# Kernel optimization log

Measured on AMD Instinct MI355X. Metric: run time of the kernel, lower is better.

Reference implementation:

```python
import jax, jax.numpy as jnp
import numpy as np

B, H, W = 16, 180, 240  # dim=(180,240), batch inferred from last event in torch code
N = 8_000_000


def setup_inputs() -> dict:
    key = jax.random.key(0)
    k0, k1, k2, k3, k4 = jax.random.split(key, 5)
    x = jax.random.randint(k0, (N,), 0, W).astype(jnp.float32)
    y = jax.random.randint(k1, (N,), 0, H).astype(jnp.float32)
    t = jax.random.uniform(k2, (N,), dtype=jnp.float32)
    p = (jax.random.randint(k3, (N,), 0, 2) * 2 - 1).astype(jnp.float32)  # polarity in {-1,1}
    # b sorted so events[-1,-1] == B-1, matching how torch code infers B
    b = jnp.sort(jax.random.randint(k4, (N,), 0, B)).astype(jnp.float32)
    events = jnp.stack([x, y, t, p, b], axis=1)  # [N,5]
    return {"events": events}


def reference(events):
    x, y, t, p, b = (events[:, i] for i in range(5))
    bi = b.astype(jnp.int32)

    # per-batch time normalization: t /= max(t within batch)
    tmax = jax.ops.segment_max(t, bi, num_segments=B)
    t = t / tmax[bi]
    p = (p + 1.0) / 2.0  # computed (as in torch) but unused downstream

    # full-res event-count histogram: idx = x + W*y + W*H*b
    idx_c = (x + W * y + W * H * b).astype(jnp.int32)
    container = jnp.zeros(B * H * W, jnp.int32).at[idx_c].add(1, mode="drop")
    container = container.reshape(B, H, W)

    # half-res counter/timer; replicate torch float floordiv exactly:
    # idx = x//2 + (W*y)//4 + (W*H*b)//4
    idx_k = (jnp.floor_divide(x, 2.0)
             + jnp.floor_divide(W * y, 4.0)
             + jnp.floor_divide(W * H * b, 4.0)).astype(jnp.int32)
    nvox = B * (H // 2) * (W // 2)
    counter = jnp.zeros(nvox, jnp.int32).at[idx_k].add(1, mode="drop").astype(jnp.float32)
    timer = jnp.zeros(nvox, jnp.float32).at[idx_k].add(t, mode="drop")
    timer = timer / jnp.where(counter == 0, 1.0, counter)  # mean timestamp per voxel
    counter = counter.reshape(B, H // 2, W // 2)
    timer = timer.reshape(B, H // 2, W // 2)

    # strided diffs on the full-res histogram
    dy = container[:, ::2] - container[:, 1::2]          # [B, H/2, W]
    diff_y = dy[:, :, ::2] + dy[:, :, 1::2]              # [B, H/2, W/2]
    dx = container[:, :, ::2] - container[:, :, 1::2]    # [B, H, W/2]
    diff_x = dx[:, 1::2] + dx[:, ::2]                    # [B, H/2, W/2]

    return container, counter, timer, diff_x, diff_y
```

## Files before the change

### kernel.cpp

```cpp
#include <hip/hip_runtime.h>
#include <stdint.h>

constexpr int NB    = 16;
constexpr int NH    = 180;
constexpr int NW    = 240;
constexpr int FULL  = NB * NH * NW;
constexpr int SEG   = (NH / 2) * (NW / 2);
constexpr int HALF  = NB * SEG;
constexpr int CELLS = NH * NW;
constexpr int H4W   = CELLS / 8;
constexpr int EVT   = 512;
constexpr int NBPB  = 32;
constexpr int NBLK  = NB * NBPB;
constexpr int RT    = 43;

constexpr int O_TMAX  = 0;
constexpr int O_CONT  = 16;
constexpr int O_TSUM  = O_CONT + FULL;
constexpr int O_BLEED = O_TSUM + HALF;
constexpr int ZERO_WORDS = O_BLEED + HALF;
constexpr int O_BND   = ZERO_WORDS;
constexpr int O_PRIV  = O_BND + 32;
constexpr int O_CNTFB = ZERO_WORDS;

__global__ __launch_bounds__(256) void k_init(unsigned int* __restrict__ ws, int bound) {
    int i = blockIdx.x * blockDim.x + threadIdx.x;
    int stride = gridDim.x * blockDim.x;
    for (; i < bound; i += stride) ws[i] = 0u;
}

__global__ __launch_bounds__(64) void k_bounds(const float* __restrict__ ev, int n,
                                               int* __restrict__ bnd) {
    int b = threadIdx.x;
    if (b > NB) return;
    int lo = 0, hi = n;
    while (lo < hi) {
        int mid = (lo + hi) >> 1;
        float v = ev[(size_t)5 * mid + 4];
        if (v < (float)b) lo = mid + 1; else hi = mid;
    }
    bnd[b] = lo;
}

__global__ __launch_bounds__(EVT) void k_merged(const float* __restrict__ ev,
                                                const int* __restrict__ bnd,
                                                unsigned int* __restrict__ ws,
                                                unsigned int* __restrict__ h4p,
                                                float* __restrict__ tsp) {
    unsigned int* tmaxb   = ws + O_TMAX;
    float*        bleed_g = (float*)(ws + O_BLEED);

    __shared__ unsigned int h4[H4W];
    __shared__ float        ts[SEG];
    __shared__ unsigned int bsm;
    int tid = threadIdx.x;
    for (int i = tid; i < H4W; i += EVT) h4[i] = 0u;
    for (int i = tid; i < SEG; i += EVT) ts[i] = 0.0f;
    if (tid == 0) bsm = 0u;

    int b0 = blockIdx.x >> 5;
    int r  = blockIdx.x & (NBPB - 1);
    int sb = bnd[b0], eb = bnd[b0 + 1];
    long long len = (long long)(eb - sb);
    int s = sb + (int)(len * r / NBPB);
    int e = sb + (int)(len * (r + 1) / NBPB);
    __syncthreads();

    float tloc = 0.0f;

    auto proc = [&](float fx, float fy, float t) {
        int xi = (int)fx, yi = (int)fy;
        int cell = xi + NW * yi;
        int loc  = (xi >> 1) + (NW / 4) * yi;
        tloc = fmaxf(tloc, t);
        atomicAdd(&h4[cell >> 3], 1u << ((cell & 7) * 4));
        if (loc < SEG) {
            atomicAdd(&ts[loc], t);
        } else {
            int ik = SEG * b0 + loc;
            if (ik < HALF) atomicAdd(&bleed_g[ik], t);
        }
    };

    if (s < e) {
        int as_ = min((s + 3) & ~3, e);
        for (int i = s + tid; i < as_; i += EVT) {
            const float* rr = ev + (size_t)5 * i;
            proc(rr[0], rr[1], rr[2]);
        }
        int ng = (e - as_) >> 2;
        const float4* e4 = (const float4*)ev;
        size_t qbase = (size_t)5 * (size_t)(as_ >> 2);
        for (int g = tid; g < ng; g += 2 * EVT) {
            int g2 = g + EVT;
            size_t qb = qbase + (size_t)5 * g;
            float4 q0 = e4[qb], q1 = e4[qb + 1], q2 = e4[qb + 2],
                   q3 = e4[qb + 3], q4 = e4[qb + 4];
            if (g2 < ng) {
                size_t qc = qbase + (size_t)5 * g2;
                float4 p0 = e4[qc], p1 = e4[qc + 1], p2 = e4[qc + 2],
                       p3 = e4[qc + 3], p4 = e4[qc + 4];
                proc(q0.x, q0.y, q0.z);
                proc(q1.y, q1.z, q1.w);
                proc(q2.z, q2.w, q3.x);
                proc(q3.w, q4.x, q4.y);
                proc(p0.x, p0.y, p0.z);
                proc(p1.y, p1.z, p1.w);
                proc(p2.z, p2.w, p3.x);
                proc(p3.w, p4.x, p4.y);
            } else {
                proc(q0.x, q0.y, q0.z);
                proc(q1.y, q1.z, q1.w);
                proc(q2.z, q2.w, q3.x);
                proc(q3.w, q4.x, q4.y);
            }
        }
        for (int i = as_ + (ng << 2) + tid; i < e; i += EVT) {
            const float* rr = ev + (size_t)5 * i;
            proc(rr[0], rr[1], rr[2]);
        }
    }

#pragma unroll
    for (int o = 32; o > 0; o >>= 1) tloc = fmaxf(tloc, __shfl_xor(tloc, o));
    if ((tid & 63) == 0) atomicMax(&bsm, __float_as_uint(tloc));
    __syncthreads();

    unsigned int* dh = h4p + (size_t)blockIdx.x * H4W;
    for (int i = tid; i < H4W; i += EVT) dh[i] = h4[i];
    float* dt = tsp + (size_t)blockIdx.x * SEG;
    for (int i = tid; i < SEG; i += EVT) dt[i] = ts[i];
    if (tid == 0 && bsm) atomicMax(&tmaxb[b0], bsm);
}

__global__ __launch_bounds__(256) void k_reduce(const unsigned int* __restrict__ ws,
                                                const unsigned int* __restrict__ h4p,
                                                const float* __restrict__ tsp,
                                                float* __restrict__ out) {
    const unsigned int* tmaxb   = ws + O_TMAX;
    const float*        bleed_g = (const float*)(ws + O_BLEED);

    int tid  = threadIdx.x;
    int b    = blockIdx.x / RT;
    int tile = blockIdx.x - b * RT;

    int rem = tile * 256 + tid;
    if (rem >= SEG) return;
    int v = b * SEG + rem;
    int i = rem / (NW / 2);
    int j = rem - i * (NW / 2);
    int cbl = 480 * i + 2 * j;
    int cbg = CELLS * b + cbl;

    unsigned c00 = 0, c01 = 0, c10 = 0, c11 = 0, oc = 0;
    float tsum = 0.0f;

    bool prev = false;
    int ocell;
    if (j >= 60)      ocell = cbl + 120;
    else if (i >= 1)  ocell = cbl - 120;
    else { prev = true; ocell = 43080 + 2 * j; }

    int w0i = cbl >> 3, nib = (cbl & 7) * 4;
    int w1i = w0i + 30;
    int owi = ocell >> 3, onib = (ocell & 7) * 4;

    int base = b << 5;
#pragma unroll 8
    for (int k = 0; k < NBPB; ++k) {
        const unsigned int* hp = h4p + (size_t)(base + k) * H4W;
        unsigned w0 = hp[w0i], w1 = hp[w1i], wo = hp[owi];
        float tv = tsp[(size_t)(base + k) * SEG + rem];
        c00 += (w0 >> nib) & 15u;  c01 += (w0 >> (nib + 4)) & 15u;
        c10 += (w1 >> nib) & 15u;  c11 += (w1 >> (nib + 4)) & 15u;
        oc  += ((wo >> onib) & 15u) + ((wo >> (onib + 4)) & 15u);
        tsum += tv;
    }
    if (prev) {
        oc = 0;
        if (b >= 1) {
            int pb = (b - 1) << 5;
#pragma unroll 8
            for (int k = 0; k < NBPB; ++k) {
                unsigned wo = h4p[(size_t)(pb + k) * H4W + owi];
                oc += ((wo >> onib) & 15u) + ((wo >> (onib + 4)) & 15u);
            }
        }
    }
    unsigned cnt = c00 + c01 + oc;

    out[cbg]          = (float)c00;
    out[cbg + 1]      = (float)c01;
    out[cbg + NW]     = (float)c10;
    out[cbg + NW + 1] = (float)c11;
    out[FULL + v] = (float)cnt;

    float tm = __uint_as_float(tmaxb[b]);
    if (!(tm > 0.0f)) tm = 1.0f;
    float tmp = (b > 0) ? __uint_as_float(tmaxb[b - 1]) : 1.0f;
    if (!(tmp > 0.0f)) tmp = 1.0f;
    float s = tsum / tm + bleed_g[v] / tmp;
    out[FULL + HALF + v] = s / (float)(cnt == 0 ? 1u : cnt);

    out[FULL + 2 * HALF + v] = (float)((int)c00 - (int)c01 + (int)c10 - (int)c11);
    out[FULL + 3 * HALF + v] = (float)((int)c00 + (int)c01 - (int)c10 - (int)c11);
}


__global__ __launch_bounds__(256) void f_events(const float* __restrict__ ev, int n,
                                                unsigned int* __restrict__ ws) {
    unsigned int* tmaxb = ws + O_TMAX;
    int*   cont  = (int*)(ws + O_CONT);
    int*   cnt   = (int*)(ws + O_CNTFB + 32);
    float* tsum  = (float*)(ws + O_TSUM);
    float* bleed = (float*)(ws + O_BLEED);
    __shared__ unsigned int smax[NB];
    if (threadIdx.x < NB) smax[threadIdx.x] = 0u;
    __syncthreads();
    int chunk = (n + gridDim.x - 1) / (int)gridDim.x;
    int start = blockIdx.x * chunk;
    int end   = min(start + chunk, n);
    for (int i = start + (int)threadIdx.x; i < end; i += (int)blockDim.x) {
        const float* r = ev + (size_t)5 * (size_t)i;
        int xi = (int)r[0], yi = (int)r[1], bi = (int)r[4];
        float t = r[2];
        atomicMax(&smax[bi], __float_as_uint(t));
        atomicAdd(&cont[xi + NW * yi + CELLS * bi], 1);
        int loc = (xi >> 1) + (NW / 4) * yi;
        int ik  = loc + SEG * bi;
        if (ik < HALF) {
            atomicAdd(&cnt[ik], 1);
            if (loc >= SEG) atomicAdd(&bleed[ik], t);
            else            atomicAdd(&tsum[ik], t);
        }
    }
    __syncthreads();
    if (threadIdx.x < NB) {
        unsigned v = smax[threadIdx.x];
        if (v) atomicMax(&tmaxb[threadIdx.x], v);
    }
}

__global__ __launch_bounds__(256) void f_epilogue(const unsigned int* __restrict__ ws,
                                                  float* __restrict__ out) {
    const unsigned int* tmaxb = ws + O_TMAX;
    const int*   cont  = (const int*)(ws + O_CONT);
    const int*   cnt   = (const int*)(ws + O_CNTFB + 32);
    const float* tsum  = (const float*)(ws + O_TSUM);
    const float* bleed = (const float*)(ws + O_BLEED);
    int v = blockIdx.x * blockDim.x + threadIdx.x;
    if (v >= HALF) return;
    int b   = v / SEG;
    int rem = v - b * SEG;
    int i   = rem / (NW / 2);
    int j   = rem - i * (NW / 2);
    int cbase = b * CELLS + 480 * i + 2 * j;
    int c00 = cont[cbase],      c01 = cont[cbase + 1];
    int c10 = cont[cbase + NW], c11 = cont[cbase + NW + 1];
    out[cbase]          = (float)c00;
    out[cbase + 1]      = (float)c01;
    out[cbase + NW]     = (float)c10;
    out[cbase + NW + 1] = (float)c11;
    int c = cnt[v];
    out[FULL + v] = (float)c;
    float tm  = __uint_as_float(tmaxb[b]);
    if (!(tm > 0.0f)) tm = 1.0f;
    float tmp = (b > 0) ? __uint_as_float(tmaxb[b - 1]) : 1.0f;
    if (!(tmp > 0.0f)) tmp = 1.0f;
    float s   = tsum[v] / tm + bleed[v] / tmp;
    out[FULL + HALF + v] = s / (float)(c == 0 ? 1 : c);
    out[FULL + 2 * HALF + v] = (float)(c00 - c01 + c10 - c11);
    out[FULL + 3 * HALF + v] = (float)(c00 + c01 - c10 - c11);
}

extern "C" void kernel_launch(void* const* d_in, const int* in_sizes, int n_in,
                              void* d_out, int out_size, void* d_ws, size_t ws_size,
                              hipStream_t stream) {
    const float* ev = (const float*)d_in[0];
    int n = in_sizes[0] / 5;
    unsigned int* ws = (unsigned int*)d_ws;
    float* out = (float*)d_out;

    size_t need = (size_t)(O_PRIV + NBLK * (H4W + SEG)) * 4u;

    if (ws_size >= need && n > 0) {
        unsigned int* h4p = ws + O_PRIV;
        float*        tsp = (float*)(ws + O_PRIV + NBLK * H4W);
        int*          bnd = (int*)(ws + O_BND);
        hipLaunchKernelGGL(k_init, dim3(512), dim3(256), 0, stream, ws, ZERO_WORDS);
        hipLaunchKernelGGL(k_bounds, dim3(1), dim3(64), 0, stream, ev, n, bnd);
        hipLaunchKernelGGL(k_merged, dim3(NBLK), dim3(EVT), 0, stream, ev, bnd, ws, h4p, tsp);
        hipLaunchKernelGGL(k_reduce, dim3(NB * RT), dim3(256), 0, stream, ws, h4p, tsp, out);
    } else {
        hipLaunchKernelGGL(k_init, dim3(512), dim3(256), 0, stream, ws, ZERO_WORDS + 32 + HALF);
        hipLaunchKernelGGL(f_events, dim3(2048), dim3(256), 0, stream, ev, n, ws);
        hipLaunchKernelGGL(f_epilogue, dim3((HALF + 255) / 256), dim3(256), 0, stream, ws, out);
    }
}
```

Baseline: 256.8 us.

## Shrink zeroed workspace, fuse bounds search into init, and stage bleed atomics in LDS

The workspace is reordered so the fast path only zeroes tmax and the bleed array instead of the full container and tsum buffers, and the init kernel now runs the per-batch binary search itself, which removes one launch. Overflowing half-res indices are accumulated in a padded shared timer array and flushed with at most 60 global atomics per block, replacing per-event global atomics. The event kernel block size doubles to 1024 threads and the reduce loops are unrolled further. The larger block may lower occupancy, and the fused search runs in block 0 while the other blocks do the zeroing.

```diff
diff --git a/kernel.cpp b/kernel.cpp
--- a/kernel.cpp
+++ b/kernel.cpp
@@ -9,53 +9,53 @@
 constexpr int HALF  = NB * SEG;
 constexpr int CELLS = NH * NW;
 constexpr int H4W   = CELLS / 8;
-constexpr int EVT   = 512;
+constexpr int EVT   = 1024;
 constexpr int NBPB  = 32;
 constexpr int NBLK  = NB * NBPB;
 constexpr int RT    = 43;
+constexpr int TSX   = SEG + 60;
 
 constexpr int O_TMAX  = 0;
-constexpr int O_CONT  = 16;
-constexpr int O_TSUM  = O_CONT + FULL;
-constexpr int O_BLEED = O_TSUM + HALF;
-constexpr int ZERO_WORDS = O_BLEED + HALF;
-constexpr int O_BND   = ZERO_WORDS;
+constexpr int O_BLEED = 16;
+constexpr int ZFAST   = O_BLEED + HALF;
+constexpr int O_BND   = ZFAST;
 constexpr int O_PRIV  = O_BND + 32;
-constexpr int O_CNTFB = ZERO_WORDS;
-
-__global__ __launch_bounds__(256) void k_init(unsigned int* __restrict__ ws, int bound) {
-    int i = blockIdx.x * blockDim.x + threadIdx.x;
-    int stride = gridDim.x * blockDim.x;
+constexpr int O_CONT  = O_PRIV;
+constexpr int O_TSUMF = O_CONT + FULL;
+constexpr int O_CNTFB = O_TSUMF + HALF;
+constexpr int ZFALL   = O_CNTFB + HALF;
+
+__global__ __launch_bounds__(256) void k_init(unsigned int* __restrict__ ws, int bound,
+                                              const float* __restrict__ ev, int n) {
+    int tid = threadIdx.x;
+    int i = blockIdx.x * 256 + tid;
+    int stride = gridDim.x * 256;
     for (; i < bound; i += stride) ws[i] = 0u;
-}
-
-__global__ __launch_bounds__(64) void k_bounds(const float* __restrict__ ev, int n,
-                                               int* __restrict__ bnd) {
-    int b = threadIdx.x;
-    if (b > NB) return;
-    int lo = 0, hi = n;
-    while (lo < hi) {
-        int mid = (lo + hi) >> 1;
-        float v = ev[(size_t)5 * mid + 4];
-        if (v < (float)b) lo = mid + 1; else hi = mid;
-    }
-    bnd[b] = lo;
+    if (blockIdx.x == 0 && tid <= NB) {
+        int lo = 0, hi = n;
+        while (lo < hi) {
+            int mid = (lo + hi) >> 1;
+            float v = ev[(size_t)5 * mid + 4];
+            if (v < (float)tid) lo = mid + 1; else hi = mid;
+        }
+        ((int*)(ws + O_BND))[tid] = lo;
+    }
 }
 
 __global__ __launch_bounds__(EVT) void k_merged(const float* __restrict__ ev,
-                                                const int* __restrict__ bnd,
                                                 unsigned int* __restrict__ ws,
                                                 unsigned int* __restrict__ h4p,
                                                 float* __restrict__ tsp) {
     unsigned int* tmaxb   = ws + O_TMAX;
     float*        bleed_g = (float*)(ws + O_BLEED);
+    const int*    bnd     = (const int*)(ws + O_BND);
 
     __shared__ unsigned int h4[H4W];
-    __shared__ float        ts[SEG];
+    __shared__ float        ts[TSX];
     __shared__ unsigned int bsm;
     int tid = threadIdx.x;
     for (int i = tid; i < H4W; i += EVT) h4[i] = 0u;
-    for (int i = tid; i < SEG; i += EVT) ts[i] = 0.0f;
+    for (int i = tid; i < TSX; i += EVT) ts[i] = 0.0f;
     if (tid == 0) bsm = 0u;
 
     int b0 = blockIdx.x >> 5;
@@ -74,12 +74,7 @@
         int loc  = (xi >> 1) + (NW / 4) * yi;
         tloc = fmaxf(tloc, t);
         atomicAdd(&h4[cell >> 3], 1u << ((cell & 7) * 4));
-        if (loc < SEG) {
-            atomicAdd(&ts[loc], t);
-        } else {
-            int ik = SEG * b0 + loc;
-            if (ik < HALF) atomicAdd(&bleed_g[ik], t);
-        }
+        atomicAdd(&ts[loc], t);
     };
 
     if (s < e) {
@@ -130,6 +125,10 @@
     for (int i = tid; i < H4W; i += EVT) dh[i] = h4[i];
     float* dt = tsp + (size_t)blockIdx.x * SEG;
     for (int i = tid; i < SEG; i += EVT) dt[i] = ts[i];
+    if (b0 < NB - 1 && tid < 60) {
+        float v = ts[SEG + tid];
+        if (v != 0.0f) atomicAdd(&bleed_g[(b0 + 1) * SEG + tid], v);
+    }
     if (tid == 0 && bsm) atomicMax(&tmaxb[b0], bsm);
 }
 
@@ -166,7 +165,7 @@
     int owi = ocell >> 3, onib = (ocell & 7) * 4;
 
     int base = b << 5;
-#pragma unroll 8
+#pragma unroll 16
     for (int k = 0; k < NBPB; ++k) {
         const unsigned int* hp = h4p + (size_t)(base + k) * H4W;
         unsigned w0 = hp[w0i], w1 = hp[w1i], wo = hp[owi];
@@ -180,7 +179,7 @@
         oc = 0;
         if (b >= 1) {
             int pb = (b - 1) << 5;
-#pragma unroll 8
+#pragma unroll 16
             for (int k = 0; k < NBPB; ++k) {
                 unsigned wo = h4p[(size_t)(pb + k) * H4W + owi];
                 oc += ((wo >> onib) & 15u) + ((wo >> (onib + 4)) & 15u);
@@ -211,8 +210,8 @@
                                                 unsigned int* __restrict__ ws) {
     unsigned int* tmaxb = ws + O_TMAX;
     int*   cont  = (int*)(ws + O_CONT);
-    int*   cnt   = (int*)(ws + O_CNTFB + 32);
-    float* tsum  = (float*)(ws + O_TSUM);
+    int*   cnt   = (int*)(ws + O_CNTFB);
+    float* tsum  = (float*)(ws + O_TSUMF);
     float* bleed = (float*)(ws + O_BLEED);
     __shared__ unsigned int smax[NB];
     if (threadIdx.x < NB) smax[threadIdx.x] = 0u;
@@ -245,8 +244,8 @@
                                                   float* __restrict__ out) {
     const unsigned int* tmaxb = ws + O_TMAX;
     const int*   cont  = (const int*)(ws + O_CONT);
-    const int*   cnt   = (const int*)(ws + O_CNTFB + 32);
-    const float* tsum  = (const float*)(ws + O_TSUM);
+    const int*   cnt   = (const int*)(ws + O_CNTFB);
+    const float* tsum  = (const float*)(ws + O_TSUMF);
     const float* bleed = (const float*)(ws + O_BLEED);
     int v = blockIdx.x * blockDim.x + threadIdx.x;
     if (v >= HALF) return;
@@ -286,13 +285,11 @@
     if (ws_size >= need && n > 0) {
         unsigned int* h4p = ws + O_PRIV;
         float*        tsp = (float*)(ws + O_PRIV + NBLK * H4W);
-        int*          bnd = (int*)(ws + O_BND);
-        hipLaunchKernelGGL(k_init, dim3(512), dim3(256), 0, stream, ws, ZERO_WORDS);
-        hipLaunchKernelGGL(k_bounds, dim3(1), dim3(64), 0, stream, ev, n, bnd);
-        hipLaunchKernelGGL(k_merged, dim3(NBLK), dim3(EVT), 0, stream, ev, bnd, ws, h4p, tsp);
+        hipLaunchKernelGGL(k_init, dim3(64), dim3(256), 0, stream, ws, ZFAST, ev, n);
+        hipLaunchKernelGGL(k_merged, dim3(NBLK), dim3(EVT), 0, stream, ev, ws, h4p, tsp);
         hipLaunchKernelGGL(k_reduce, dim3(NB * RT), dim3(256), 0, stream, ws, h4p, tsp, out);
     } else {
-        hipLaunchKernelGGL(k_init, dim3(512), dim3(256), 0, stream, ws, ZERO_WORDS + 32 + HALF);
+        hipLaunchKernelGGL(k_init, dim3(512), dim3(256), 0, stream, ws, ZFALL, ev, n);
         hipLaunchKernelGGL(f_events, dim3(2048), dim3(256), 0, stream, ev, n, ws);
         hipLaunchKernelGGL(f_epilogue, dim3((HALF + 255) / 256), dim3(256), 0, stream, ws, out);
     }
```

New measurement: 255.1 us. No clear change (-0.7%).
